# Kernel optimization log

Hardware: AMD Instinct MI355X
Metric: run time of the kernel (lower is better)

Reference implementation:

```python
import jax, jax.numpy as jnp
import numpy as np
import math

DIM, HEADS, COMPRESS = 2048, 16, 8
HEAD_DIM = DIM // HEADS          # 128
HALF = HEAD_DIM // 2             # 64 (Q/K head dim after low-rank up-proj)
LATENT = DIM // COMPRESS         # 256
B, S = 2, 2048


def setup_inputs() -> dict:
    key = jax.random.key(0)
    ks = jax.random.split(key, 7)
    sc = lambda fan_in: 1.0 / math.sqrt(fan_in)
    return {
        "x": jax.random.normal(ks[0], (B, S, DIM), jnp.float32),
        "wq_d": jax.random.normal(ks[1], (DIM, LATENT), jnp.float32) * sc(DIM),
        "wkv_d": jax.random.normal(ks[2], (DIM, LATENT), jnp.float32) * sc(DIM),
        "wq_u": jax.random.normal(ks[3], (LATENT, HEADS * HALF), jnp.float32) * sc(LATENT),
        "wk_u": jax.random.normal(ks[4], (LATENT, HEADS * HALF), jnp.float32) * sc(LATENT),
        "wv_u": jax.random.normal(ks[5], (LATENT, DIM), jnp.float32) * sc(LATENT),
        "wo": jax.random.normal(ks[6], (DIM, DIM), jnp.float32) * sc(DIM),
    }


def _rope_tables(seq_len):
    # LlamaRotaryEmbedding with dim = HALF
    inv_freq = 1.0 / (10000.0 ** (jnp.arange(0, HALF, 2, dtype=jnp.float32) / HALF))  # [HALF//2]
    t = jnp.arange(seq_len, dtype=jnp.float32)
    freqs = t[:, None] * inv_freq[None, :]          # [S, HALF//2]
    emb = jnp.concatenate([freqs, freqs], axis=-1)  # [S, HALF]
    cos = jnp.cos(emb)[None, :, None, :]            # [1, S, 1, HALF]
    sin = jnp.sin(emb)[None, :, None, :]
    return cos, sin


def _rotate_half(x):
    x1, x2 = jnp.split(x, 2, axis=-1)
    return jnp.concatenate([-x2, x1], axis=-1)


def reference(x, wq_d, wkv_d, wq_u, wk_u, wv_u, wo):
    b, s, d = x.shape
    q_latent = x @ wq_d                      # [B,S,LATENT]
    kv_latent = x @ wkv_d                    # [B,S,LATENT]
    q = (q_latent @ wq_u).reshape(b, s, HEADS, HALF)
    k = (kv_latent @ wk_u).reshape(b, s, HEADS, HALF)
    v = (kv_latent @ wv_u).reshape(b, s, HEADS, HEAD_DIM)

    cos, sin = _rope_tables(s)
    q = q * cos + _rotate_half(q) * sin
    k = k * cos + _rotate_half(k) * sin

    scale = 1.0 / math.sqrt(HALF)
    attn = jnp.einsum("bqhd,bkhd->bhqk", q, k) * scale   # [B,H,S,S] (no mask, as in source)
    attn = jax.nn.softmax(attn, axis=-1)
    out = jnp.einsum("bhqk,bkhd->bqhd", attn, v)         # [B,S,H,HEAD_DIM]
    out = out.reshape(b, s, d)
    return out @ wo
```

## Files before the change

kernel.cpp:

```cpp
#include <hip/hip_runtime.h>
#include <stdint.h>

typedef unsigned short u16;
typedef __attribute__((ext_vector_type(8))) short bf16x8;
typedef __attribute__((ext_vector_type(4))) float f32x4;
typedef __attribute__((ext_vector_type(4))) unsigned short u16x4;

#define DIM 2048
#define HEADS 16
#define HEAD_DIM 128
#define HALF 64
#define LATENT 256
#define BATCH 2
#define SEQ 2048
#define TOK (BATCH*SEQ)

#if defined(__has_builtin)
#if __has_builtin(__builtin_amdgcn_exp2f)
#define EXP2F(x) __builtin_amdgcn_exp2f(x)
#endif
#endif
#ifndef EXP2F
#define EXP2F(x) exp2f(x)
#endif

#define SCALE_C 0.18033688011112042f

__device__ __forceinline__ u16 f2bf(float f) {
  uint32_t u = __float_as_uint(f);
  u += 0x7fff + ((u >> 16) & 1);
  return (u16)(u >> 16);
}

__device__ __forceinline__ f32x4 mfma16(bf16x8 a, bf16x8 b, f32x4 c) {
  return __builtin_amdgcn_mfma_f32_16x16x32_bf16(a, b, c, 0, 0, 0);
}

__device__ __forceinline__ void async_copy16(const void* g, void* l) {
  __builtin_amdgcn_global_load_lds(
      (const __attribute__((address_space(1))) void*)g,
      (__attribute__((address_space(3))) void*)l, 16, 0, 0);
}

__global__ void prep_k(const float* __restrict__ wq_d, const float* __restrict__ wkv_d,
                       const float* __restrict__ wq_u, const float* __restrict__ wk_u,
                       const float* __restrict__ wv_u, const float* __restrict__ wo,
                       u16* __restrict__ wdT, u16* __restrict__ wquT, u16* __restrict__ wkuT,
                       u16* __restrict__ wvuT, u16* __restrict__ woT,
                       float* __restrict__ ct, float* __restrict__ st) {
  __shared__ float tile[32][33];
  const int f = blockIdx.x;
  const int tx = threadIdx.x, ty = threadIdx.y;

  const float* in = nullptr;
  u16* out = nullptr;
  int N = 0, row_off = 0, out_ld = 0, bx = 0, by = 0;

  if (f < 1024) {
    int z = f >> 9, r = f & 511;
    bx = r & 7; by = r >> 3;
    in = z ? wkv_d : wq_d; out = wdT; row_off = z * 256; N = 256; out_ld = 2048;
  } else if (f < 1536) {
    int r = f - 1024; int z = r >> 8; r &= 255;
    bx = r & 31; by = r >> 5;
    in = z ? wk_u : wq_u; out = z ? wkuT : wquT; row_off = 0; N = 1024; out_ld = 256;
  } else if (f < 2048) {
    int r = f - 1536;
    bx = r & 63; by = r >> 6;
    in = wv_u; out = wvuT; row_off = 0; N = 2048; out_ld = 256;
  } else if (f < 6144) {
    int r = f - 2048;
    bx = r & 63; by = r >> 6;
    in = wo; out = woT; row_off = 0; N = 2048; out_ld = 2048;
  } else {
    int t = (f - 6144) * 256 + ty * 32 + tx;
    int i = t & 31, s = t >> 5;
    float invf = expf(-(float)i * 0.28782313662425575f);
    float a = (float)s * invf;
    ct[t] = cosf(a);
    st[t] = sinf(a);
    return;
  }
  int k0 = by * 32, n0 = bx * 32;
  #pragma unroll
  for (int j = 0; j < 32; j += 8)
    tile[ty + j][tx] = in[(size_t)(k0 + ty + j) * N + n0 + tx];
  __syncthreads();
  #pragma unroll
  for (int j = 0; j < 32; j += 8)
    out[(size_t)(n0 + ty + j + row_off) * out_ld + k0 + tx] = f2bf(tile[tx][ty + j]);
}

template<int NS, int OUTF32>
__global__ void combine_k(const float* __restrict__ p, void* __restrict__ out, int n4, int slab4) {
  int t = blockIdx.x * 256 + threadIdx.x;
  if (t >= n4) return;
  float4 a = ((const float4*)p)[t];
  #pragma unroll
  for (int s = 1; s < NS; ++s) {
    float4 b = ((const float4*)p)[t + (size_t)s * slab4];
    a.x += b.x; a.y += b.y; a.z += b.z; a.w += b.w;
  }
  if (OUTF32) ((float4*)out)[t] = a;
  else { u16x4 o = { f2bf(a.x), f2bf(a.y), f2bf(a.z), f2bf(a.w) };
         *(u16x4*)((u16*)out + (size_t)t * 4) = o; }
}

template<int MODE>
__global__ __launch_bounds__(256)
void gemm_bt(const u16* __restrict__ A, int lda, int a_off,
             const u16* __restrict__ BT, int ldb,
             void* __restrict__ Cv, int M, int N, int K) {
  __shared__ __align__(16) u16 As[128 * 32];
  __shared__ __align__(16) u16 Bs[128 * 32];
  const int tid = threadIdx.x;
  const int lane = tid & 63;
  const int wid = tid >> 6;
  const int z = blockIdx.z;
  int koff = z * K;
  const int nb = gridDim.x * gridDim.y;
  int f = blockIdx.x + gridDim.x * blockIdx.y;
  f = (f & 7) * (nb >> 3) + (f >> 3);
  const int m0 = (f / gridDim.x) * 128;
  const int n0 = (f % gridDim.x) * 128;
  const int wr = wid >> 1, wc = wid & 1;
  const int l15 = lane & 15, lg = lane >> 4;
  const int rA = lane >> 2;
  const int kqL = (lane & 3) * 8;
  const int kqS = ((((lane & 3) - ((lane >> 3) & 3)) & 3)) * 8;
  const int sWr = (((lane & 3) + ((lane >> 3) & 3)) & 3) * 8;
  const int rsw = (l15 >> 1) & 3;

  f32x4 acc[4][4] = {};
  const int nk = K / 32;
  for (int kt = 0; kt < nk; ++kt) {
    const int k0 = koff + kt * 32;
    #pragma unroll
    for (int c = 0; c < 2; ++c) {
      int ca = wid * 2 + c;
      if (MODE == 5) {
        const float* Af = (const float*)A;
        const float* ga = Af + (size_t)(m0 + ca * 16 + rA) * lda + a_off + k0 + kqL;
        float4 v0 = *(const float4*)ga;
        float4 v1 = *(const float4*)(ga + 4);
        union { u16 h[8]; bf16x8 v; } pk;
        pk.h[0] = f2bf(v0.x); pk.h[1] = f2bf(v0.y); pk.h[2] = f2bf(v0.z); pk.h[3] = f2bf(v0.w);
        pk.h[4] = f2bf(v1.x); pk.h[5] = f2bf(v1.y); pk.h[6] = f2bf(v1.z); pk.h[7] = f2bf(v1.w);
        *(bf16x8*)&As[ca * 512 + rA * 32 + sWr] = pk.v;
      } else {
        const u16* ga = A + (size_t)(m0 + ca * 16 + rA) * lda + a_off + k0 + kqS;
        async_copy16(ga, &As[ca * 512]);
      }
      const u16* gb = BT + (size_t)(n0 + ca * 16 + rA) * ldb + k0 + kqS;
      async_copy16(gb, &Bs[ca * 512]);
    }
    __syncthreads();
    bf16x8 af[4], bfr[4];
    #pragma unroll
    for (int i = 0; i < 4; ++i) {
      af[i]  = *(const bf16x8*)&As[(wr * 64 + i * 16 + l15) * 32 + (((lg + rsw) & 3) * 8)];
      bfr[i] = *(const bf16x8*)&Bs[(wc * 64 + i * 16 + l15) * 32 + (((lg + rsw) & 3) * 8)];
    }
    #pragma unroll
    for (int i = 0; i < 4; ++i)
      #pragma unroll
      for (int j = 0; j < 4; ++j)
        acc[i][j] = mfma16(af[i], bfr[j], acc[i][j]);
    __syncthreads();
  }
  #pragma unroll
  for (int i = 0; i < 4; ++i) {
    #pragma unroll
    for (int j = 0; j < 4; ++j) {
      int row = m0 + wr * 64 + i * 16 + lg * 4;
      int col = n0 + wc * 64 + j * 16 + l15;
      #pragma unroll
      for (int r = 0; r < 4; ++r)
        ((float*)Cv)[(size_t)z * M * N + (size_t)(row + r) * N + col] = acc[i][j][r];
    }
  }
}

__global__ __launch_bounds__(256)
void upproj_k(const u16* __restrict__ A,
              const u16* __restrict__ wquT, const u16* __restrict__ wkuT,
              const u16* __restrict__ wvuT,
              u16* __restrict__ qb, u16* __restrict__ kb, u16* __restrict__ vT,
              const float* __restrict__ ct, const float* __restrict__ st) {
  __shared__ __align__(16) u16 As[128 * 32];
  __shared__ __align__(16) u16 Bs[128 * 32];
  const int tid = threadIdx.x;
  const int lane = tid & 63;
  const int wid = tid >> 6;
  int f = blockIdx.x;
  f = (f & 7) * 128 + (f >> 3);
  const u16* BT; u16* out; int N, a_off, seg, r;
  if (f < 256)      { seg = 0; r = f;       BT = wquT; out = qb; N = 1024; a_off = 0; }
  else if (f < 512) { seg = 1; r = f - 256; BT = wkuT; out = kb; N = 1024; a_off = 256; }
  else              { seg = 2; r = f - 512; BT = wvuT; out = vT; N = 2048; a_off = 256; }
  const int gx = (seg == 2) ? 16 : 8;
  const int m0 = (r / gx) * 128;
  const int n0 = (r % gx) * 128;
  const int wr = wid >> 1, wc = wid & 1;
  const int l15 = lane & 15, lg = lane >> 4;
  const int rA = lane >> 2;
  const int kqS = ((((lane & 3) - ((lane >> 3) & 3)) & 3)) * 8;
  const int rsw = (l15 >> 1) & 3;

  f32x4 acc[4][4] = {};
  for (int kt = 0; kt < LATENT / 32; ++kt) {
    const int k0 = kt * 32;
    #pragma unroll
    for (int c = 0; c < 2; ++c) {
      int ca = wid * 2 + c;
      async_copy16(A + (size_t)(m0 + ca * 16 + rA) * 512 + a_off + k0 + kqS, &As[ca * 512]);
      async_copy16(BT + (size_t)(n0 + ca * 16 + rA) * LATENT + k0 + kqS, &Bs[ca * 512]);
    }
    __syncthreads();
    bf16x8 af[4], bfr[4];
    #pragma unroll
    for (int i = 0; i < 4; ++i) {
      af[i]  = *(const bf16x8*)&As[(wr * 64 + i * 16 + l15) * 32 + (((lg + rsw) & 3) * 8)];
      bfr[i] = *(const bf16x8*)&Bs[(wc * 64 + i * 16 + l15) * 32 + (((lg + rsw) & 3) * 8)];
    }
    #pragma unroll
    for (int i = 0; i < 4; ++i)
      #pragma unroll
      for (int j = 0; j < 4; ++j)
        acc[i][j] = mfma16(af[i], bfr[j], acc[i][j]);
    __syncthreads();
  }

  if (seg <= 1) {
    const float qs = seg ? 1.0f : SCALE_C;
    #pragma unroll
    for (int i = 0; i < 4; ++i) {
      int rowb = m0 + wr * 64 + i * 16 + lg * 4;
      #pragma unroll
      for (int j = 0; j < 2; ++j) {
        int ii = j * 16 + l15;
        int colb = n0 + wc * 64;
        #pragma unroll
        for (int r2 = 0; r2 < 4; ++r2) {
          int s = (rowb + r2) & (SEQ - 1);
          float c = ct[s * 32 + ii], sn = st[s * 32 + ii];
          float x1 = acc[i][j][r2], x2 = acc[i][j + 2][r2];
          out[(size_t)(rowb + r2) * N + colb + ii]      = f2bf((x1 * c - x2 * sn) * qs);
          out[(size_t)(rowb + r2) * N + colb + ii + 32] = f2bf((x2 * c + x1 * sn) * qs);
        }
      }
    }
  } else {
    const int bb = m0 >> 11;
    #pragma unroll
    for (int i = 0; i < 4; ++i) {
      int rowb = m0 + wr * 64 + i * 16 + lg * 4;
      int s = rowb & (SEQ - 1);
      int pbase = (s & ~31) + (((s & 15) >> 2) << 3) + (((s >> 4) & 1) << 2);
      #pragma unroll
      for (int j = 0; j < 4; ++j) {
        int c = n0 + wc * 64 + j * 16 + l15;
        u16x4 ov = { f2bf(acc[i][j][0]), f2bf(acc[i][j][1]),
                     f2bf(acc[i][j][2]), f2bf(acc[i][j][3]) };
        *(u16x4*)&out[(size_t)bb * SEQ * DIM + (size_t)c * SEQ + pbase] = ov;
      }
    }
  }
}

#define KVB 64
__global__ __launch_bounds__(256, 2)
void attn_kernel(const u16* __restrict__ Q, const u16* __restrict__ Kb,
                 const u16* __restrict__ VT, u16* __restrict__ O) {
  __shared__ __align__(16) u16 Ks[3][KVB * 64];
  __shared__ __align__(16) u16 Vs[3][HEAD_DIM * KVB];

  const int tid = threadIdx.x, lane = tid & 63, wid = tid >> 6;
  int fl = blockIdx.x + 16 * (blockIdx.y + 16 * blockIdx.z);
  fl = (fl & 7) * 64 + (fl >> 3);
  const int q0 = (fl & 15) * 128;
  const int h = (fl >> 4) & 15;
  const int b = fl >> 8;
  const int l15 = lane & 15, lg = lane >> 4;

  const u16* kbp = Kb + (size_t)(b * SEQ) * (HEADS * HALF) + h * HALF;
  const u16* vtb = VT + (size_t)b * SEQ * DIM + (size_t)(h * HEAD_DIM) * SEQ;

  bf16x8 qf[2][2];
  #pragma unroll
  for (int m = 0; m < 2; ++m)
    #pragma unroll
    for (int ks = 0; ks < 2; ++ks)
      qf[m][ks] = *(const bf16x8*)&Q[(size_t)(b * SEQ + q0 + wid * 32 + m * 16 + l15) * (HEADS * HALF)
                                     + h * HALF + ks * 32 + lg * 8];

  f32x4 o[2][8] = {};
  float l_part[2] = {0.f, 0.f};

  const int row8 = lane >> 3;
  const int colB = ((lane & 7) ^ row8) * 16;

  auto stage = [&](u16* KsD, u16* VsD, int kv0) {
    #pragma unroll
    for (int i = 0; i < 2; ++i) {
      int c = wid * 2 + i;
      const u16* src = kbp + (size_t)(kv0 + c * 8 + row8) * (HEADS * HALF) + (colB >> 1);
      async_copy16(src, KsD + c * 512);
    }
    #pragma unroll
    for (int i = 0; i < 4; ++i) {
      int c = wid * 4 + i;
      const u16* src = vtb + (size_t)(c * 8 + row8) * SEQ + kv0 + (colB >> 1);
      async_copy16(src, VsD + c * 512);
    }
  };

  auto compute = [&](const u16* KsP, const u16* VsP) {
    const char* KsB = (const char*)KsP;
    const char* VsB = (const char*)VsP;
    const int kswz = (l15 & 7) << 4;
    bf16x8 kf[2][4];
    #pragma unroll
    for (int ks = 0; ks < 2; ++ks)
      #pragma unroll
      for (int nf = 0; nf < 4; ++nf)
        kf[ks][nf] = *(const bf16x8*)(KsB + (nf * 16 + l15) * 128 + ((ks * 64 + lg * 16) ^ kswz));
    f32x4 s[2][4] = {};
    __builtin_amdgcn_s_setprio(1);
    #pragma unroll
    for (int ks = 0; ks < 2; ++ks)
      #pragma unroll
      for (int nf = 0; nf < 4; ++nf) {
        s[0][nf] = mfma16(kf[ks][nf], qf[0][ks], s[0][nf]);
        s[1][nf] = mfma16(kf[ks][nf], qf[1][ks], s[1][nf]);
      }
    __builtin_amdgcn_s_setprio(0);
    #pragma unroll
    for (int ks2 = 0; ks2 < 2; ++ks2) {
      bf16x8 vf[8];
      #pragma unroll
      for (int db = 0; db < 8; ++db) {
        int row = db * 16 + l15;
        vf[db] = *(const bf16x8*)(VsB + row * 128 + ((ks2 * 64 + lg * 16) ^ ((row & 7) << 4)));
      }
      bf16x8 pa[2];
      #pragma unroll
      for (int m = 0; m < 2; ++m) {
        float p[8];
        #pragma unroll
        for (int nf2 = 0; nf2 < 2; ++nf2)
          #pragma unroll
          for (int r = 0; r < 4; ++r) {
            float v = EXP2F(s[m][ks2 * 2 + nf2][r]);
            p[nf2 * 4 + r] = v;
            l_part[m] += v;
          }
        union { uint32_t u[4]; bf16x8 v8; } pk;
        asm("v_cvt_pk_bf16_f32 %0, %1, %2" : "=v"(pk.u[0]) : "v"(p[0]), "v"(p[1]));
        asm("v_cvt_pk_bf16_f32 %0, %1, %2" : "=v"(pk.u[1]) : "v"(p[2]), "v"(p[3]));
        asm("v_cvt_pk_bf16_f32 %0, %1, %2" : "=v"(pk.u[2]) : "v"(p[4]), "v"(p[5]));
        asm("v_cvt_pk_bf16_f32 %0, %1, %2" : "=v"(pk.u[3]) : "v"(p[6]), "v"(p[7]));
        pa[m] = pk.v8;
      }
      __builtin_amdgcn_s_setprio(1);
      #pragma unroll
      for (int db = 0; db < 8; ++db) {
        o[0][db] = mfma16(pa[0], vf[db], o[0][db]);
        o[1][db] = mfma16(pa[1], vf[db], o[1][db]);
      }
      __builtin_amdgcn_s_setprio(0);
    }
  };

#define WAIT6 asm volatile("s_waitcnt vmcnt(6)" ::: "memory")
#define WAIT0 asm volatile("s_waitcnt vmcnt(0)" ::: "memory")
#define BAR   __builtin_amdgcn_s_barrier()

  stage(Ks[0], Vs[0], 0);
  stage(Ks[1], Vs[1], KVB);
  WAIT6; BAR;
  int t = 0;
  for (int i = 0; i < 10; ++i) {
    stage(Ks[2], Vs[2], (t + 2) * KVB); compute(Ks[0], Vs[0]); WAIT6; BAR;
    stage(Ks[0], Vs[0], (t + 3) * KVB); compute(Ks[1], Vs[1]); WAIT6; BAR;
    stage(Ks[1], Vs[1], (t + 4) * KVB); compute(Ks[2], Vs[2]); WAIT6; BAR;
    t += 3;
  }
  compute(Ks[0], Vs[0]); WAIT0; BAR;
  compute(Ks[1], Vs[1]);

#undef WAIT6
#undef WAIT0
#undef BAR

  #pragma unroll
  for (int m = 0; m < 2; ++m) {
    float l = l_part[m];
    l += __shfl_xor(l, 16);
    l += __shfl_xor(l, 32);
    float inv[4];
    #pragma unroll
    for (int r = 0; r < 4; ++r)
      inv[r] = 1.0f / __shfl(l, lg * 4 + r);
    #pragma unroll
    for (int db = 0; db < 8; ++db)
      #pragma unroll
      for (int r = 0; r < 4; ++r) {
        int row = q0 + wid * 32 + m * 16 + lg * 4 + r;
        O[(size_t)(b * SEQ + row) * DIM + h * HEAD_DIM + db * 16 + l15] = f2bf(o[m][db][r] * inv[r]);
      }
  }
}

extern "C" void kernel_launch(void* const* d_in, const int* in_sizes, int n_in,
                              void* d_out, int out_size, void* d_ws, size_t ws_size,
                              hipStream_t stream) {
  const float* x     = (const float*)d_in[0];
  const float* wq_d  = (const float*)d_in[1];
  const float* wkv_d = (const float*)d_in[2];
  const float* wq_u  = (const float*)d_in[3];
  const float* wk_u  = (const float*)d_in[4];
  const float* wv_u  = (const float*)d_in[5];
  const float* wo    = (const float*)d_in[6];

  char* ws = (char*)d_ws;
  size_t off = 0;
  auto alloc = [&](size_t bytes) -> void* {
    void* p = ws + off;
    off += (bytes + 255) & ~(size_t)255;
    return p;
  };
  u16* wdT    = (u16*)alloc((size_t)512 * DIM * 2);
  u16* wquT   = (u16*)alloc((size_t)1024 * LATENT * 2);
  u16* wkuT   = (u16*)alloc((size_t)1024 * LATENT * 2);
  u16* wvuT   = (u16*)alloc((size_t)DIM * LATENT * 2);
  u16* woT    = (u16*)alloc((size_t)DIM * DIM * 2);
  u16* lat    = (u16*)alloc((size_t)TOK * 512 * 2);
  float* latP = (float*)alloc((size_t)4 * TOK * 512 * 4);
  u16* qb     = (u16*)alloc((size_t)TOK * 1024 * 2);
  u16* kb     = (u16*)alloc((size_t)TOK * 1024 * 2);
  u16* vT     = (u16*)alloc((size_t)TOK * DIM * 2);
  u16* ao     = (u16*)alloc((size_t)TOK * DIM * 2);
  float* ct   = (float*)alloc((size_t)SEQ * 32 * 4);
  float* st   = (float*)alloc((size_t)SEQ * 32 * 4);
  (void)in_sizes; (void)n_in; (void)out_size; (void)ws_size;

  prep_k<<<dim3(6400), dim3(32, 8), 0, stream>>>(wq_d, wkv_d, wq_u, wk_u, wv_u, wo,
                                                 wdT, wquT, wkuT, wvuT, woT, ct, st);

  gemm_bt<5><<<dim3(4, 32, 4), 256, 0, stream>>>((const u16*)x, DIM, 0, wdT, DIM, latP, TOK, 512, 512);
  combine_k<4, 0><<<(TOK * 512 / 4 + 255) / 256, 256, 0, stream>>>(latP, lat, TOK * 512 / 4, TOK * 512 / 4);

  upproj_k<<<dim3(1024), 256, 0, stream>>>(lat, wquT, wkuT, wvuT, qb, kb, vT, ct, st);

  attn_kernel<<<dim3(SEQ / 128, HEADS, BATCH), 256, 0, stream>>>(qb, kb, vT, ao);

  gemm_bt<3><<<dim3(16, 32, 1), 256, 0, stream>>>(ao, DIM, 0, woT, DIM, (float*)d_out, TOK, DIM, DIM);
}
```

Before: 165.3 us.

## Add triple-buffered async-copy pipeline to output projection GEMM

Splits the templated GEMM into a latent-projection kernel and a dedicated output-projection kernel. The output projection now uses three LDS buffers with async global-to-LDS copies issued two tiles ahead. It waits with a partial vmcnt and a single barrier per K-step, and raises wave priority around the MFMA block. This is meant to hide global load latency and halve the barrier count. In exchange it triples LDS use per block, which may reduce occupancy, and hardcodes the K loop to DIM.

Measured after the change: 157.6 us. -4.6%, faster.

```diff
diff --git a/kernel.cpp b/kernel.cpp
--- a/kernel.cpp
+++ b/kernel.cpp
@@ -106,11 +106,9 @@
          *(u16x4*)((u16*)out + (size_t)t * 4) = o; }
 }
 
-template<int MODE>
 __global__ __launch_bounds__(256)
-void gemm_bt(const u16* __restrict__ A, int lda, int a_off,
-             const u16* __restrict__ BT, int ldb,
-             void* __restrict__ Cv, int M, int N, int K) {
+void gemm_lat(const float* __restrict__ A, int lda, const u16* __restrict__ BT, int ldb,
+              float* __restrict__ Cv, int M, int N, int K) {
   __shared__ __align__(16) u16 As[128 * 32];
   __shared__ __align__(16) u16 Bs[128 * 32];
   const int tid = threadIdx.x;
@@ -138,28 +136,23 @@
     #pragma unroll
     for (int c = 0; c < 2; ++c) {
       int ca = wid * 2 + c;
-      if (MODE == 5) {
-        const float* Af = (const float*)A;
-        const float* ga = Af + (size_t)(m0 + ca * 16 + rA) * lda + a_off + k0 + kqL;
-        float4 v0 = *(const float4*)ga;
-        float4 v1 = *(const float4*)(ga + 4);
-        union { u16 h[8]; bf16x8 v; } pk;
-        pk.h[0] = f2bf(v0.x); pk.h[1] = f2bf(v0.y); pk.h[2] = f2bf(v0.z); pk.h[3] = f2bf(v0.w);
-        pk.h[4] = f2bf(v1.x); pk.h[5] = f2bf(v1.y); pk.h[6] = f2bf(v1.z); pk.h[7] = f2bf(v1.w);
-        *(bf16x8*)&As[ca * 512 + rA * 32 + sWr] = pk.v;
-      } else {
-        const u16* ga = A + (size_t)(m0 + ca * 16 + rA) * lda + a_off + k0 + kqS;
-        async_copy16(ga, &As[ca * 512]);
-      }
+      const float* ga = A + (size_t)(m0 + ca * 16 + rA) * lda + k0 + kqL;
+      float4 v0 = *(const float4*)ga;
+      float4 v1 = *(const float4*)(ga + 4);
+      union { u16 h[8]; bf16x8 v; } pk;
+      pk.h[0] = f2bf(v0.x); pk.h[1] = f2bf(v0.y); pk.h[2] = f2bf(v0.z); pk.h[3] = f2bf(v0.w);
+      pk.h[4] = f2bf(v1.x); pk.h[5] = f2bf(v1.y); pk.h[6] = f2bf(v1.z); pk.h[7] = f2bf(v1.w);
+      *(bf16x8*)&As[ca * 512 + rA * 32 + sWr] = pk.v;
       const u16* gb = BT + (size_t)(n0 + ca * 16 + rA) * ldb + k0 + kqS;
       async_copy16(gb, &Bs[ca * 512]);
     }
     __syncthreads();
     bf16x8 af[4], bfr[4];
+    const int slot = ((lg + rsw) & 3) * 8;
     #pragma unroll
     for (int i = 0; i < 4; ++i) {
-      af[i]  = *(const bf16x8*)&As[(wr * 64 + i * 16 + l15) * 32 + (((lg + rsw) & 3) * 8)];
-      bfr[i] = *(const bf16x8*)&Bs[(wc * 64 + i * 16 + l15) * 32 + (((lg + rsw) & 3) * 8)];
+      af[i]  = *(const bf16x8*)&As[(wr * 64 + i * 16 + l15) * 32 + slot];
+      bfr[i] = *(const bf16x8*)&Bs[(wc * 64 + i * 16 + l15) * 32 + slot];
     }
     #pragma unroll
     for (int i = 0; i < 4; ++i)
@@ -176,7 +169,87 @@
       int col = n0 + wc * 64 + j * 16 + l15;
       #pragma unroll
       for (int r = 0; r < 4; ++r)
-        ((float*)Cv)[(size_t)z * M * N + (size_t)(row + r) * N + col] = acc[i][j][r];
+        Cv[(size_t)z * M * N + (size_t)(row + r) * N + col] = acc[i][j][r];
+    }
+  }
+}
+
+__global__ __launch_bounds__(256)
+void gemm_wo(const u16* __restrict__ A, const u16* __restrict__ BT,
+             float* __restrict__ C) {
+  __shared__ __align__(16) u16 As[3][128 * 32];
+  __shared__ __align__(16) u16 Bs[3][128 * 32];
+  const int tid = threadIdx.x, lane = tid & 63, wid = tid >> 6;
+  const int nb = gridDim.x * gridDim.y;
+  int f = blockIdx.x + gridDim.x * blockIdx.y;
+  f = (f & 7) * (nb >> 3) + (f >> 3);
+  const int m0 = (f / gridDim.x) * 128;
+  const int n0 = (f % gridDim.x) * 128;
+  const int wr = wid >> 1, wc = wid & 1;
+  const int l15 = lane & 15, lg = lane >> 4;
+  const int rA = lane >> 2;
+  const int kqS = ((((lane & 3) - ((lane >> 3) & 3)) & 3)) * 8;
+  const int rsw = (l15 >> 1) & 3;
+
+  f32x4 acc[4][4] = {};
+
+  auto stage = [&](u16* AsD, u16* BsD, int k0) {
+    #pragma unroll
+    for (int c = 0; c < 2; ++c) {
+      int ca = wid * 2 + c;
+      async_copy16(A + (size_t)(m0 + ca * 16 + rA) * DIM + k0 + kqS, AsD + ca * 512);
+      async_copy16(BT + (size_t)(n0 + ca * 16 + rA) * DIM + k0 + kqS, BsD + ca * 512);
+    }
+  };
+  auto compute = [&](const u16* AsP, const u16* BsP) {
+    bf16x8 af[4], bfr[4];
+    const int slot = ((lg + rsw) & 3) * 8;
+    #pragma unroll
+    for (int i = 0; i < 4; ++i) {
+      af[i]  = *(const bf16x8*)&AsP[(wr * 64 + i * 16 + l15) * 32 + slot];
+      bfr[i] = *(const bf16x8*)&BsP[(wc * 64 + i * 16 + l15) * 32 + slot];
+    }
+    __builtin_amdgcn_s_setprio(1);
+    #pragma unroll
+    for (int i = 0; i < 4; ++i)
+      #pragma unroll
+      for (int j = 0; j < 4; ++j)
+        acc[i][j] = mfma16(af[i], bfr[j], acc[i][j]);
+    __builtin_amdgcn_s_setprio(0);
+  };
+
+#define WAIT4 asm volatile("s_waitcnt vmcnt(4)" ::: "memory")
+#define WAIT0 asm volatile("s_waitcnt vmcnt(0)" ::: "memory")
+#define BAR   __builtin_amdgcn_s_barrier()
+
+  stage(As[0], Bs[0], 0);
+  stage(As[1], Bs[1], 32);
+  WAIT4; BAR;
+  int t = 0;
+  for (int i = 0; i < 20; ++i) {
+    stage(As[2], Bs[2], (t + 2) * 32); compute(As[0], Bs[0]); WAIT4; BAR;
+    stage(As[0], Bs[0], (t + 3) * 32); compute(As[1], Bs[1]); WAIT4; BAR;
+    stage(As[1], Bs[1], (t + 4) * 32); compute(As[2], Bs[2]); WAIT4; BAR;
+    t += 3;
+  }
+  stage(As[2], Bs[2], 62 * 32); compute(As[0], Bs[0]); WAIT4; BAR;
+  stage(As[0], Bs[0], 63 * 32); compute(As[1], Bs[1]); WAIT4; BAR;
+  compute(As[2], Bs[2]); WAIT0; BAR;
+  compute(As[0], Bs[0]);
+
+#undef WAIT4
+#undef WAIT0
+#undef BAR
+
+  #pragma unroll
+  for (int i = 0; i < 4; ++i) {
+    #pragma unroll
+    for (int j = 0; j < 4; ++j) {
+      int row = m0 + wr * 64 + i * 16 + lg * 4;
+      int col = n0 + wc * 64 + j * 16 + l15;
+      #pragma unroll
+      for (int r = 0; r < 4; ++r)
+        C[(size_t)(row + r) * DIM + col] = acc[i][j][r];
     }
   }
 }
@@ -218,10 +291,11 @@
     }
     __syncthreads();
     bf16x8 af[4], bfr[4];
+    const int slot = ((lg + rsw) & 3) * 8;
     #pragma unroll
     for (int i = 0; i < 4; ++i) {
-      af[i]  = *(const bf16x8*)&As[(wr * 64 + i * 16 + l15) * 32 + (((lg + rsw) & 3) * 8)];
-      bfr[i] = *(const bf16x8*)&Bs[(wc * 64 + i * 16 + l15) * 32 + (((lg + rsw) & 3) * 8)];
+      af[i]  = *(const bf16x8*)&As[(wr * 64 + i * 16 + l15) * 32 + slot];
+      bfr[i] = *(const bf16x8*)&Bs[(wc * 64 + i * 16 + l15) * 32 + slot];
     }
     #pragma unroll
     for (int i = 0; i < 4; ++i)
@@ -448,12 +522,12 @@
   prep_k<<<dim3(6400), dim3(32, 8), 0, stream>>>(wq_d, wkv_d, wq_u, wk_u, wv_u, wo,
                                                  wdT, wquT, wkuT, wvuT, woT, ct, st);
 
-  gemm_bt<5><<<dim3(4, 32, 4), 256, 0, stream>>>((const u16*)x, DIM, 0, wdT, DIM, latP, TOK, 512, 512);
+  gemm_lat<<<dim3(4, 32, 4), 256, 0, stream>>>(x, DIM, wdT, DIM, latP, TOK, 512, 512);
   combine_k<4, 0><<<(TOK * 512 / 4 + 255) / 256, 256, 0, stream>>>(latP, lat, TOK * 512 / 4, TOK * 512 / 4);
 
   upproj_k<<<dim3(1024), 256, 0, stream>>>(lat, wquT, wkuT, wvuT, qb, kb, vT, ct, st);
 
   attn_kernel<<<dim3(SEQ / 128, HEADS, BATCH), 256, 0, stream>>>(qb, kb, vT, ao);
 
-  gemm_bt<3><<<dim3(16, 32, 1), 256, 0, stream>>>(ao, DIM, 0, woT, DIM, (float*)d_out, TOK, DIM, DIM);
-}
+  gemm_wo<<<dim3(16, 32), 256, 0, stream>>>(ao, woT, (float*)d_out);
+}
```
